# Kernel optimization log

Measured on AMD Instinct MI355X. Metric: run time of the kernel, lower is better.

## Reference

```python
import jax, jax.numpy as jnp
import numpy as np

K = 10  # module init kwarg k; Kmin selects k+1 then drops the self-distance column


def setup_inputs() -> dict:
    key = jax.random.key(0)
    N, D = 16384, 512
    obs = jax.random.normal(key, (N, D), dtype=jnp.float32)
    return {"obs": obs}


def reference(obs):
    # sa_ent=False -> x = y = obs
    x = obs
    # (same math as ((x_i - y_j)**2).sum(), expressed as a dense GEMM)
    sq = jnp.sum(x * x, axis=-1)  # [N]
    d2 = sq[:, None] + sq[None, :] - 2.0 * (x @ x.T)  # [N, N]
    # k+1 smallest per row (self-distance 0 included), ascending order
    neg_vals, _ = jax.lax.top_k(-d2, K + 1)  # [N, K+1]
    smallest = -neg_vals
    # drop self column, clamp tiny negatives from the expansion, sqrt
    r = jnp.sqrt(jnp.maximum(smallest[:, 1:], 0.0))  # [N, K]
    # style == 'log_mean'
    return jnp.log1p(jnp.mean(r, axis=-1))  # [N]
```

## Files before the change

kernel.cpp:

```cpp
#include <hip/hip_runtime.h>
#include <math.h>

#define NPTS 16384
#define DIM  512
#define KSEL 11
#define NSPLIT 4
#define CPS   (NPTS / NSPLIT)
#define BM    128
#define BN    64
#define MITERS (CPS / BN)
#define TITERS 16
#define STRIPB 8192
#define CAP   48
#define QS    22.0f

typedef __attribute__((ext_vector_type(4))) int i32x4;

__device__ __forceinline__ void gload_lds16(const void* g, void* l) {
    __builtin_amdgcn_global_load_lds(
        (const __attribute__((address_space(1))) void*)g,
        (__attribute__((address_space(3))) void*)l, 16, 0, 0);
}

__device__ __forceinline__ void pinreg(i32x4& v) { asm volatile("" : "+v"(v)); }
__device__ __forceinline__ void pini(int& v)     { asm volatile("" : "+v"(v)); }

__device__ __forceinline__ int topk_scan_i(const int* v, int n, int* a) {
    #pragma unroll
    for (int p = 0; p < KSEL; ++p) a[p] = v[p];
    int mx = a[0];
    #pragma unroll
    for (int p = 1; p < KSEL; ++p) mx = max(mx, a[p]);
    for (int i = KSEL; i < n; ++i) {
        const int x = v[i];
        if (x < mx) {
            bool done = false;
            #pragma unroll
            for (int p = 0; p < KSEL; ++p) {
                const bool rep = (!done) && (a[p] == mx);
                a[p] = rep ? x : a[p];
                done = done || rep;
            }
            mx = a[0];
            #pragma unroll
            for (int p = 1; p < KSEL; ++p) mx = max(mx, a[p]);
        }
    }
    return mx;
}

__global__ void prep_convert(const float* __restrict__ obs, char* __restrict__ obsb,
                             int* __restrict__ sqi) {
    const int wv = threadIdx.x >> 6, ln = threadIdx.x & 63;
    const int row = blockIdx.x * 4 + wv;
    const float4* s = (const float4*)(obs + (unsigned long)row * DIM + ln * 8);
    const float4 a = s[0], b = s[1];
    float xs[8] = {a.x, a.y, a.z, a.w, b.x, b.y, b.z, b.w};
    unsigned long u = 0ul;
    int ssum = 0;
    #pragma unroll
    for (int j = 0; j < 8; ++j) {
        const int q = __float2int_rn(fminf(fmaxf(xs[j] * QS, -127.f), 127.f));
        ssum += q * q;
        u |= ((unsigned long)((unsigned)q & 0xffu)) << (8 * j);
    }
    *(unsigned long*)(obsb + (unsigned long)(row >> 4) * STRIPB + (ln >> 3) * 1024
                      + ((ln >> 1) & 3) * 256 + (row & 15) * 16 + (ln & 1) * 8) = u;
    #pragma unroll
    for (int off = 32; off; off >>= 1) ssum += __shfl_xor(ssum, off);
    if (ln == 0) sqi[row] = ssum;
}

#define STAGE(BUF, CITER) do {                                                  \
        const char* gs_ = obsb + (unsigned long)((C0 >> 4) + 4 * (CITER)) * STRIPB \
                          + wv * 8192 + ln * 16;                                \
        char* lb_ = &Braw[BUF][0] + wv * 8192;                                  \
        _Pragma("unroll")                                                       \
        for (int r_ = 0; r_ < 8; ++r_)                                          \
            gload_lds16(gs_ + r_ * 1024, lb_ + r_ * 1024);                      \
    } while (0)

#define GEMM_BODY(CUR, CITER)                                                   \
        const char* bp = &Braw[CUR][0];                                         \
        i32x4 acc[2][4] = {{{0,0,0,0},{0,0,0,0},{0,0,0,0},{0,0,0,0}},           \
                           {{0,0,0,0},{0,0,0,0},{0,0,0,0},{0,0,0,0}}};          \
        _Pragma("unroll")                                                       \
        for (int cg = 0; cg < 4; ++cg) {                                        \
            _Pragma("unroll")                                                   \
            for (int t = 0; t < 8; ++t) {                                       \
                const i32x4 b = *(const i32x4*)(bp + cg * STRIPB + t * 1024 + lfrag); \
                acc[0][cg] = __builtin_amdgcn_mfma_i32_16x16x64_i8(b, afrag[0][t], acc[0][cg], 0, 0, 0); \
                acc[1][cg] = __builtin_amdgcn_mfma_i32_16x16x64_i8(b, afrag[1][t], acc[1][cg], 0, 0, 0); \
            }                                                                   \
        }                                                                       \
        i32x4 sqv[4];                                                           \
        _Pragma("unroll")                                                       \
        for (int cg_ = 0; cg_ < 4; ++cg_)                                       \
            sqv[cg_] = *(const i32x4*)(sqi + C0 + (CITER) * BN + cg_ * 16 + kc * 4);

#define DIST(S, CG, R) (sqr[S] + sqv[CG][R] - 2 * acc[S][CG][R])

#define LOAD_AFRAG() do {                                                       \
        _Pragma("unroll")                                                       \
        for (int s = 0; s < 2; ++s) {                                           \
            const unsigned long sbase = (unsigned long)((R0 >> 4) + wv * 2 + s) * STRIPB; \
            _Pragma("unroll")                                                   \
            for (int t = 0; t < 8; ++t) {                                       \
                afrag[s][t] = *(const i32x4*)(obsb + sbase + t * 1024 + lfrag); \
                pinreg(afrag[s][t]);                                            \
            }                                                                   \
            sqr[s] = sqi[wrow0 + s * 16 + lr];                                  \
            pini(sqr[s]);                                                       \
        }                                                                       \
    } while (0)

__global__ __launch_bounds__(256, 2) void thresh_pass(
    const char* __restrict__ obsb, const int* __restrict__ sqi,
    int* __restrict__ Tv)
{
    __shared__ __align__(16) char Braw[2][BN * 512];

    const int tid = threadIdx.x;
    const int wv = tid >> 6, ln = tid & 63;
    const int q  = blockIdx.x >> 7;
    const int rt = blockIdx.x & 127;
    const int R0 = rt * BM;
    const int C0 = q * CPS;
    const int wrow0 = R0 + wv * 32;
    const int lr = ln & 15;
    const int kc = ln >> 4;
    const int lfrag = kc * 256 + lr * 16;

    i32x4 afrag[2][8];
    int sqr[2];
    LOAD_AFRAG();

    int segmin[2][16];
    #pragma unroll
    for (int s = 0; s < 2; ++s)
        #pragma unroll
        for (int p = 0; p < 16; ++p) segmin[s][p] = 0x7FFFFFFF;

    STAGE(0, 0);
    __syncthreads();
    #pragma unroll 2
    for (int it = 0; it < TITERS; ++it) {
        const int cur = it & 1;
        if (it + 1 < TITERS) STAGE(cur ^ 1, it + 1);
        GEMM_BODY(cur, it);
        #pragma unroll
        for (int s = 0; s < 2; ++s)
            #pragma unroll
            for (int cg = 0; cg < 4; ++cg)
                #pragma unroll
                for (int r = 0; r < 4; ++r)
                    segmin[s][cg * 4 + r] = min(segmin[s][cg * 4 + r], DIST(s, cg, r));
        __syncthreads();
    }

    int* mins = (int*)&Braw[0][0];
    #pragma unroll
    for (int s = 0; s < 2; ++s)
        #pragma unroll
        for (int p = 0; p < 16; ++p)
            mins[(wv * 32 + s * 16 + lr) * 65 + kc * 16 + p] = segmin[s][p];
    __syncthreads();
    if (tid < BM) {
        int a[KSEL];
        topk_scan_i(mins + tid * 65, 64, a);
        #pragma unroll
        for (int p = 0; p < KSEL; ++p)
            Tv[(unsigned long)(R0 + tid) * (4 * KSEL) + q * KSEL + p] = a[p];
    }
}

__global__ void tmerge(const int* __restrict__ Tv, int* __restrict__ T) {
    const int row = blockIdx.x * 256 + threadIdx.x;
    int a[KSEL];
    T[row] = topk_scan_i(Tv + (unsigned long)row * (4 * KSEL), 4 * KSEL, a);
}

__global__ __launch_bounds__(256, 2) void knn_main(
    const char* __restrict__ obsb, const int* __restrict__ sqi,
    const int* __restrict__ T, int* __restrict__ cnt,
    int* __restrict__ vals)
{
    __shared__ __align__(16) char Braw[2][BN * 512];
    __shared__ unsigned lcnt[BM];

    const int tid = threadIdx.x;
    const int wv = tid >> 6, ln = tid & 63;
    const int sp = blockIdx.x >> 7;
    const int rt = blockIdx.x & 127;
    const int R0 = rt * BM;
    const int C0 = sp * CPS;
    const int wrow0 = R0 + wv * 32;
    const int lr = ln & 15;
    const int kc = ln >> 4;
    const int lfrag = kc * 256 + lr * 16;

    if (tid < BM) lcnt[tid] = 0u;

    i32x4 afrag[2][8];
    int sqr[2];
    LOAD_AFRAG();

    unsigned lrow[2]; int tval[2]; int* vbase[2];
    #pragma unroll
    for (int s = 0; s < 2; ++s) {
        const int row = wrow0 + s * 16 + lr;
        lrow[s]  = wv * 32 + s * 16 + lr;
        tval[s]  = T[row];
        pini(tval[s]);
        vbase[s] = vals + ((unsigned long)row * 4 + sp) * CAP;
    }

#define APP(S, VV) do {                                                         \
        const int v_ = (VV);                                                    \
        if (v_ <= tval[S]) {                                                    \
            const unsigned i_ = atomicAdd(&lcnt[lrow[S]], 1u);                  \
            if (i_ < CAP) vbase[S][i_] = v_;                                    \
        }                                                                       \
    } while (0)

    STAGE(0, 0);
    __syncthreads();
    #pragma unroll 2
    for (int it = 0; it < MITERS; ++it) {
        const int cur = it & 1;
        if (it + 1 < MITERS) STAGE(cur ^ 1, it + 1);
        GEMM_BODY(cur, it);
        #pragma unroll
        for (int s = 0; s < 2; ++s) {
            #pragma unroll
            for (int cg = 0; cg < 4; ++cg) {
                APP(s, DIST(s, cg, 0)); APP(s, DIST(s, cg, 1));
                APP(s, DIST(s, cg, 2)); APP(s, DIST(s, cg, 3));
            }
        }
        __syncthreads();
    }

    if (tid < BM) {
        const unsigned c = lcnt[tid];
        cnt[(unsigned long)(R0 + tid) * 4 + sp] = (int)(c < CAP ? c : CAP);
    }
}

__global__ void merge_out(const int* __restrict__ cnt, const int* __restrict__ vals,
                          float* __restrict__ out) {
    const int row = blockIdx.x * 256 + threadIdx.x;
    int arr[KSEL];
    #pragma unroll
    for (int p = 0; p < KSEL; ++p) arr[p] = 0x7FFFFFFF;
    int mx = 0x7FFFFFFF;
    for (int q = 0; q < 4; ++q) {
        const int n = min(cnt[(unsigned long)row * 4 + q], CAP);
        const int* base = vals + ((unsigned long)row * 4 + q) * CAP;
        for (int i = 0; i < n; ++i) {
            const int x = base[i];
            if (x < mx) {
                bool done = false;
                #pragma unroll
                for (int p = 0; p < KSEL; ++p) {
                    const bool rep = (!done) && (arr[p] == mx);
                    arr[p] = rep ? x : arr[p];
                    done = done || rep;
                }
                mx = arr[0];
                #pragma unroll
                for (int p = 1; p < KSEL; ++p) mx = max(mx, arr[p]);
            }
        }
    }
    int mn = arr[0];
    #pragma unroll
    for (int p = 1; p < KSEL; ++p) mn = min(mn, arr[p]);
    float ssum = 0.f;
    #pragma unroll
    for (int p = 0; p < KSEL; ++p) ssum += sqrtf((float)max(arr[p], 0));
    const float smn = sqrtf((float)max(mn, 0));
    out[row] = log1pf((ssum - smn) * (0.1f / QS));
}

extern "C" void kernel_launch(void* const* d_in, const int* in_sizes, int n_in,
                              void* d_out, int out_size, void* d_ws, size_t ws_size,
                              hipStream_t stream) {
    const float* obs = (const float*)d_in[0];
    float* out = (float*)d_out;
    char* ws = (char*)d_ws;

    char* obsb = ws;
    int*  sqi  = (int*)(ws + (size_t)NPTS * 512);
    int*  T    = sqi + NPTS;
    int*  cnt  = T + NPTS;
    int*  vals = cnt + NPTS * 4;
    int*  Tv   = vals;

    prep_convert<<<NPTS / 4, 256, 0, stream>>>(obs, obsb, sqi);
    thresh_pass<<<128 * 4, 256, 0, stream>>>(obsb, sqi, Tv);
    tmerge<<<NPTS / 256, 256, 0, stream>>>(Tv, T);
    knn_main<<<128 * NSPLIT, 256, 0, stream>>>(obsb, sqi, T, cnt, vals);
    merge_out<<<NPTS / 256, 256, 0, stream>>>(cnt, vals, out);
}
```

Baseline: 285.0 us.

## Enlarge knn_main row tile to 256 and split columns eightfold

knn_main now processes 256 rows per block (64 per wave, four 16-row strips held in registers) instead of 128, so each staged B tile in LDS feeds twice as many MFMAs. Columns are split into 8 chunks instead of 4, keeping the grid at 512 blocks, and the per-split candidate cap drops from 48 to 24. The thresh pass decouples its column chunk size (TCH) from the new split. This roughly doubles A-fragment register use per thread with launch_bounds(256,2), which risks spills or lower occupancy. The smaller cap also risks dropping true neighbours if many candidates land in one split.

```diff
diff --git a/kernel.cpp b/kernel.cpp
--- a/kernel.cpp
+++ b/kernel.cpp
@@ -4,14 +4,16 @@
 #define NPTS 16384
 #define DIM  512
 #define KSEL 11
-#define NSPLIT 4
+#define NSPLIT 8
 #define CPS   (NPTS / NSPLIT)
-#define BM    128
+#define BMM   256
+#define BMT   128
 #define BN    64
 #define MITERS (CPS / BN)
 #define TITERS 16
+#define TCH   4096
 #define STRIPB 8192
-#define CAP   48
+#define CAP   24
 #define QS    22.0f
 
 typedef __attribute__((ext_vector_type(4))) int i32x4;
@@ -124,8 +126,8 @@
     const int wv = tid >> 6, ln = tid & 63;
     const int q  = blockIdx.x >> 7;
     const int rt = blockIdx.x & 127;
-    const int R0 = rt * BM;
-    const int C0 = q * CPS;
+    const int R0 = rt * BMT;
+    const int C0 = q * TCH;
     const int wrow0 = R0 + wv * 32;
     const int lr = ln & 15;
     const int kc = ln >> 4;
@@ -165,7 +167,7 @@
         for (int p = 0; p < 16; ++p)
             mins[(wv * 32 + s * 16 + lr) * 65 + kc * 16 + p] = segmin[s][p];
     __syncthreads();
-    if (tid < BM) {
+    if (tid < BMT) {
         int a[KSEL];
         topk_scan_i(mins + tid * 65, 64, a);
         #pragma unroll
@@ -186,42 +188,44 @@
     int* __restrict__ vals)
 {
     __shared__ __align__(16) char Braw[2][BN * 512];
-    __shared__ unsigned lcnt[BM];
+    __shared__ unsigned lcnt[BMM];
 
     const int tid = threadIdx.x;
     const int wv = tid >> 6, ln = tid & 63;
-    const int sp = blockIdx.x >> 7;
-    const int rt = blockIdx.x & 127;
-    const int R0 = rt * BM;
+    const int sp = blockIdx.x >> 6;
+    const int rt = blockIdx.x & 63;
+    const int R0 = rt * BMM;
     const int C0 = sp * CPS;
-    const int wrow0 = R0 + wv * 32;
+    const int wrow0 = R0 + wv * 64;
     const int lr = ln & 15;
     const int kc = ln >> 4;
     const int lfrag = kc * 256 + lr * 16;
 
-    if (tid < BM) lcnt[tid] = 0u;
-
-    i32x4 afrag[2][8];
-    int sqr[2];
-    LOAD_AFRAG();
-
-    unsigned lrow[2]; int tval[2]; int* vbase[2];
-    #pragma unroll
-    for (int s = 0; s < 2; ++s) {
+    lcnt[tid] = 0u;
+
+    i32x4 afrag[4][8];
+    int sqr[4];
+    #pragma unroll
+    for (int s = 0; s < 4; ++s) {
+        const unsigned long sbase = (unsigned long)((R0 >> 4) + wv * 4 + s) * STRIPB;
+        #pragma unroll
+        for (int t = 0; t < 8; ++t) {
+            afrag[s][t] = *(const i32x4*)(obsb + sbase + t * 1024 + lfrag);
+            pinreg(afrag[s][t]);
+        }
+        sqr[s] = sqi[wrow0 + s * 16 + lr];
+        pini(sqr[s]);
+    }
+
+    unsigned lrow[4]; int tval[4]; int* vbase[4];
+    #pragma unroll
+    for (int s = 0; s < 4; ++s) {
         const int row = wrow0 + s * 16 + lr;
-        lrow[s]  = wv * 32 + s * 16 + lr;
+        lrow[s]  = wv * 64 + s * 16 + lr;
         tval[s]  = T[row];
         pini(tval[s]);
-        vbase[s] = vals + ((unsigned long)row * 4 + sp) * CAP;
-    }
-
-#define APP(S, VV) do {                                                         \
-        const int v_ = (VV);                                                    \
-        if (v_ <= tval[S]) {                                                    \
-            const unsigned i_ = atomicAdd(&lcnt[lrow[S]], 1u);                  \
-            if (i_ < CAP) vbase[S][i_] = v_;                                    \
-        }                                                                       \
-    } while (0)
+        vbase[s] = vals + ((unsigned long)row * NSPLIT + sp) * CAP;
+    }
 
     STAGE(0, 0);
     __syncthreads();
@@ -229,21 +233,45 @@
     for (int it = 0; it < MITERS; ++it) {
         const int cur = it & 1;
         if (it + 1 < MITERS) STAGE(cur ^ 1, it + 1);
-        GEMM_BODY(cur, it);
-        #pragma unroll
-        for (int s = 0; s < 2; ++s) {
-            #pragma unroll
-            for (int cg = 0; cg < 4; ++cg) {
-                APP(s, DIST(s, cg, 0)); APP(s, DIST(s, cg, 1));
-                APP(s, DIST(s, cg, 2)); APP(s, DIST(s, cg, 3));
+        const char* bp = &Braw[cur][0];
+        i32x4 acc[4][4];
+        #pragma unroll
+        for (int s_ = 0; s_ < 4; ++s_)
+            #pragma unroll
+            for (int c_ = 0; c_ < 4; ++c_) acc[s_][c_] = (i32x4){0, 0, 0, 0};
+        #pragma unroll
+        for (int cg = 0; cg < 4; ++cg) {
+            #pragma unroll
+            for (int t = 0; t < 8; ++t) {
+                const i32x4 b = *(const i32x4*)(bp + cg * STRIPB + t * 1024 + lfrag);
+                #pragma unroll
+                for (int s_ = 0; s_ < 4; ++s_)
+                    acc[s_][cg] = __builtin_amdgcn_mfma_i32_16x16x64_i8(
+                        b, afrag[s_][t], acc[s_][cg], 0, 0, 0);
             }
         }
+        i32x4 sqv[4];
+        #pragma unroll
+        for (int c_ = 0; c_ < 4; ++c_)
+            sqv[c_] = *(const i32x4*)(sqi + C0 + it * BN + c_ * 16 + kc * 4);
+        #pragma unroll
+        for (int s_ = 0; s_ < 4; ++s_)
+            #pragma unroll
+            for (int cg = 0; cg < 4; ++cg)
+                #pragma unroll
+                for (int r = 0; r < 4; ++r) {
+                    const int v_ = sqr[s_] + sqv[cg][r] - 2 * acc[s_][cg][r];
+                    if (v_ <= tval[s_]) {
+                        const unsigned i_ = atomicAdd(&lcnt[lrow[s_]], 1u);
+                        if (i_ < CAP) vbase[s_][i_] = v_;
+                    }
+                }
         __syncthreads();
     }
 
-    if (tid < BM) {
+    {
         const unsigned c = lcnt[tid];
-        cnt[(unsigned long)(R0 + tid) * 4 + sp] = (int)(c < CAP ? c : CAP);
+        cnt[(unsigned long)(R0 + tid) * NSPLIT + sp] = (int)(c < CAP ? c : CAP);
     }
 }
 
@@ -254,9 +282,9 @@
     #pragma unroll
     for (int p = 0; p < KSEL; ++p) arr[p] = 0x7FFFFFFF;
     int mx = 0x7FFFFFFF;
-    for (int q = 0; q < 4; ++q) {
-        const int n = min(cnt[(unsigned long)row * 4 + q], CAP);
-        const int* base = vals + ((unsigned long)row * 4 + q) * CAP;
+    for (int q = 0; q < NSPLIT; ++q) {
+        const int n = min(cnt[(unsigned long)row * NSPLIT + q], CAP);
+        const int* base = vals + ((unsigned long)row * NSPLIT + q) * CAP;
         for (int i = 0; i < n; ++i) {
             const int x = base[i];
             if (x < mx) {
@@ -294,12 +322,12 @@
     int*  sqi  = (int*)(ws + (size_t)NPTS * 512);
     int*  T    = sqi + NPTS;
     int*  cnt  = T + NPTS;
-    int*  vals = cnt + NPTS * 4;
+    int*  vals = cnt + NPTS * NSPLIT;
     int*  Tv   = vals;
 
     prep_convert<<<NPTS / 4, 256, 0, stream>>>(obs, obsb, sqi);
     thresh_pass<<<128 * 4, 256, 0, stream>>>(obsb, sqi, Tv);
     tmerge<<<NPTS / 256, 256, 0, stream>>>(Tv, T);
-    knn_main<<<128 * NSPLIT, 256, 0, stream>>>(obsb, sqi, T, cnt, vals);
+    knn_main<<<64 * NSPLIT, 256, 0, stream>>>(obsb, sqi, T, cnt, vals);
     merge_out<<<NPTS / 256, 256, 0, stream>>>(cnt, vals, out);
 }
```

Measured after the change: 267.4 us. -6.2%, faster.
